# Optimization experiments

Hardware: AMD Instinct MI355X
Metric: run time of the kernel (lower is better)

Reference implementation:

```python
import jax, jax.numpy as jnp
import numpy as np

N = 50000        # vertices
E = 1_600_000    # edges (avg degree 32)
CIN = 8          # in_channels (scalar input features)
COUT = 32        # out_channels (tangent vector channels, complex -> trailing dim 2)
R = 2            # n_corr_rings (radial profile rings)
EPS = 1e-6


def setup_inputs() -> dict:
    key = jax.random.key(0)
    ks = jax.random.split(key, 12)
    x = jax.random.normal(ks[0], (N, CIN), jnp.float32)
    edge_index = jax.random.randint(ks[1], (2, E), 0, N, dtype=jnp.int32)
    # precomputed per-edge transport * radial interpolation coefficients (re, im) per ring
    pcmp_gather = jax.random.normal(ks[2], (E, R, 2), jnp.float32)
    # TransField learned radial profile and phase offset (offset=True)
    W_rad = jax.random.normal(ks[3], (R, CIN, COUT), jnp.float32) / np.float32(np.sqrt(R * CIN))
    phase = jax.random.normal(ks[4], (COUT,), jnp.float32)
    # TangentNonLin bias after the field conv
    b_nl = jax.random.normal(ks[5], (COUT,), jnp.float32) * 0.1
    # three TangentPerceptrons: complex-linear (real weight shared over re/im) + TangentNonLin
    sc = np.float32(1.0 / np.sqrt(COUT))
    W1 = jax.random.normal(ks[6], (COUT, COUT), jnp.float32) * sc
    b1 = jax.random.normal(ks[7], (COUT,), jnp.float32) * 0.1
    W2 = jax.random.normal(ks[8], (COUT, COUT), jnp.float32) * sc
    b2 = jax.random.normal(ks[9], (COUT,), jnp.float32) * 0.1
    W3 = jax.random.normal(ks[10], (COUT, COUT), jnp.float32) * sc
    b3 = jax.random.normal(ks[11], (COUT,), jnp.float32) * 0.1
    return dict(x=x, edge_index=edge_index, pcmp_gather=pcmp_gather, W_rad=W_rad,
                phase=phase, b_nl=b_nl, W1=W1, b1=b1, W2=W2, b2=b2, W3=W3, b3=b3)


def tangent_nonlin(z, b):
    # ReLU on magnitude with learned per-channel bias, phase preserved
    mag = jnp.sqrt(jnp.sum(z * z, axis=-1) + EPS)           # [N, C]
    scale = jax.nn.relu(mag + b) / mag                      # [N, C]
    return z * scale[..., None]


def trans_field(x, src, dst, pcmp_gather, W_rad, phase, n_nodes):
    xs = x[src]                                             # gather: [E, CIN]
    t = jnp.einsum('ei,rio->ero', xs, W_rad)                # [E, R, COUT]
    # modulate by complex transport coeffs per ring, sum rings -> [E, COUT, 2]
    msg = jnp.sum(t[..., None] * pcmp_gather[:, :, None, :], axis=1)
    agg = jax.ops.segment_sum(msg, dst, num_segments=n_nodes)  # scatter: [N, COUT, 2]
    # learned phase offset: rotate each output channel by e^{i*phase}
    c, s = jnp.cos(phase), jnp.sin(phase)
    re = agg[..., 0] * c - agg[..., 1] * s
    im = agg[..., 0] * s + agg[..., 1] * c
    return jnp.stack([re, im], axis=-1)                     # [N, COUT, 2]


def reference(x, edge_index, pcmp_gather, W_rad, phase, b_nl, W1, b1, W2, b2, W3, b3):
    src, dst = edge_index[0], edge_index[1]
    y = trans_field(x, src, dst, pcmp_gather, W_rad, phase, x.shape[0])
    y = tangent_nonlin(y, b_nl)
    for W, b in ((W1, b1), (W2, b2), (W3, b3)):
        y = jnp.einsum('nik,io->nok', y, W)                 # complex-linear (shared real weight)
        y = tangent_nonlin(y, b)
    return y
```

## Files before the change

kernel.cpp:

```cpp
#include <hip/hip_runtime.h>

#define CIN 8
#define COUT 32
#define NR 2
#define EPSF 1e-6f

#define BSH 5
#define BNODES 32
#define NBMAX 2048
#define CHUNK 4096
#define BINT 512
#define BREG (CHUNK / BINT)
#define IDBITS 21
#define IDMASK ((1u << IDBITS) - 1u)
#define SRCMASK 0x03FFFFFFu
#define PSTAGE 1792
#define AREG (PSTAGE / 256)

__device__ __forceinline__ unsigned bf16r(float f) {
    unsigned u = __float_as_uint(f);
    return (u + 0x7FFFu + ((u >> 16) & 1u)) >> 16;
}
__device__ __forceinline__ unsigned pk2(float a, float b) {
    return bf16r(a) | (bf16r(b) << 16);
}
__device__ __forceinline__ float ulo(unsigned w) { return __uint_as_float(w << 16); }
__device__ __forceinline__ float uhi(unsigned w) { return __uint_as_float(w & 0xFFFF0000u); }

__global__ __launch_bounds__(256) void bucket_hist(
    const int* __restrict__ eidx, int* __restrict__ bucketCnt, int E, int nb)
{
    __shared__ int cnt[NBMAX];
    for (int i = threadIdx.x; i < nb; i += 256) cnt[i] = 0;
    __syncthreads();
    for (int e = blockIdx.x * 256 + threadIdx.x; e < E; e += gridDim.x * 256)
        atomicAdd(&cnt[eidx[E + e] >> BSH], 1);
    __syncthreads();
    for (int i = threadIdx.x; i < nb; i += 256)
        if (cnt[i]) atomicAdd(&bucketCnt[i], cnt[i]);
}

__global__ __launch_bounds__(1024) void scan_init(
    const int* __restrict__ bucketCnt, int* __restrict__ bucketBase,
    int* __restrict__ gCursor, int nb)
{
    __shared__ int sA[NBMAX], sB[NBMAX];
    for (int i = threadIdx.x; i < NBMAX; i += 1024)
        sA[i] = (i < nb) ? bucketCnt[i] : 0;
    __syncthreads();
    int* src = sA; int* dst = sB;
    for (int off = 1; off < NBMAX; off <<= 1) {
        for (int i = threadIdx.x; i < NBMAX; i += 1024)
            dst[i] = src[i] + (i >= off ? src[i - off] : 0);
        __syncthreads();
        int* tmp = src; src = dst; dst = tmp;
    }
    for (int i = threadIdx.x; i < nb; i += 1024) {
        int incl = src[i];
        int base = incl - bucketCnt[i];
        bucketBase[i] = base;
        gCursor[i] = base;
        if (i == nb - 1) bucketBase[nb] = incl;
    }
}

template<bool PACKED>
__global__ __launch_bounds__(BINT) void binify(
    const int* __restrict__ eidx, int* __restrict__ gCursor,
    unsigned* __restrict__ outMeta,
    uint2*    __restrict__ pcmpS,
    const float* __restrict__ pcmp, int E, int nb)
{
    __shared__ int cnt[NBMAX];
    __shared__ int sIncl[NBMAX];
    __shared__ int gbase[NBMAX];
    __shared__ int wsum[8];
    __shared__ unsigned sid[CHUNK];
    __shared__ unsigned short bucketOf[CHUNK];

    const int e0 = blockIdx.x * CHUNK;
    const int num = min(CHUNK, E - e0);
    const int t = threadIdx.x;
    const int lane = t & 63, wid = t >> 6;

    for (int i = t; i < nb; i += BINT) cnt[i] = 0;
    __syncthreads();

    int dreg[BREG];
#pragma unroll
    for (int kk = 0; kk < BREG; ++kk) {
        int k = t + kk * BINT;
        if (k < num) {
            dreg[kk] = eidx[E + e0 + k];
            atomicAdd(&cnt[dreg[kk] >> BSH], 1);
        }
    }
    __syncthreads();

    {
        int j0 = t * 4;
        int v0 = (j0 + 0 < nb) ? cnt[j0 + 0] : 0;
        int v1 = (j0 + 1 < nb) ? cnt[j0 + 1] : 0;
        int v2 = (j0 + 2 < nb) ? cnt[j0 + 2] : 0;
        int v3 = (j0 + 3 < nb) ? cnt[j0 + 3] : 0;
        int p0 = v0, p1 = p0 + v1, p2 = p1 + v2, p3 = p2 + v3;
        int incl = p3;
#pragma unroll
        for (int off = 1; off < 64; off <<= 1) {
            int u = __shfl_up(incl, off, 64);
            if (lane >= off) incl += u;
        }
        int laneEx = incl - p3;
        if (lane == 63) wsum[wid] = incl;
        __syncthreads();
        if (t == 0) {
            int acc = 0;
#pragma unroll
            for (int i = 0; i < 8; ++i) { int w = wsum[i]; wsum[i] = acc; acc += w; }
        }
        __syncthreads();
        int off0 = wsum[wid] + laneEx;
        sIncl[j0 + 0] = off0 + p0;
        sIncl[j0 + 1] = off0 + p1;
        sIncl[j0 + 2] = off0 + p2;
        sIncl[j0 + 3] = off0 + p3;
    }
    __syncthreads();

    for (int b = t; b < nb; b += BINT) {
        int c = sIncl[b] - (b ? sIncl[b - 1] : 0);
        gbase[b] = c ? atomicAdd(&gCursor[b], c) : 0;
    }
    __syncthreads();
    for (int i = t; i < nb; i += BINT) cnt[i] = 0;
    __syncthreads();

#pragma unroll
    for (int kk = 0; kk < BREG; ++kk) {
        int k = t + kk * BINT;
        if (k < num) {
            int e = e0 + k;
            int d = dreg[kk];
            int b = d >> BSH;
            int slot = (b ? sIncl[b - 1] : 0) + atomicAdd(&cnt[b], 1);
            sid[slot] = ((unsigned)(d & (BNODES - 1)) << IDBITS) | (unsigned)e;
            bucketOf[slot] = (unsigned short)b;
        }
    }
    __syncthreads();

    for (int s = t; s < num; s += BINT) {
        int b = bucketOf[s];
        int intra = s - (b ? sIncl[b - 1] : 0);
        unsigned v = sid[s];
        int pos = gbase[b] + intra;
        if (PACKED) {
            int id = v & IDMASK;
            unsigned dl = v >> IDBITS;
            unsigned sv = (unsigned)eidx[id];
            outMeta[pos] = (dl << 26) | sv;
            float4 pc = *reinterpret_cast<const float4*>(pcmp + (size_t)id * 4);
            uint2 pw;
            pw.x = pk2(pc.x, pc.y);
            pw.y = pk2(pc.z, pc.w);
            pcmpS[pos] = pw;
        } else {
            outMeta[pos] = v;
        }
    }
}

template<bool SRC16>
__global__ __launch_bounds__(256, 6) void fused_team_kernel(
    const float* __restrict__ x,
    const uint2* __restrict__ pcmpS,
    const unsigned* __restrict__ meta,
    const int* __restrict__ bucketBase,
    const float* __restrict__ W_rad, const float* __restrict__ phase,
    const float* __restrict__ b_nl,
    const float* __restrict__ W1, const float* __restrict__ b1,
    const float* __restrict__ W2, const float* __restrict__ b2,
    const float* __restrict__ W3, const float* __restrict__ b3,
    float* __restrict__ out, int N)
{
    __shared__ float sWrad[NR * CIN][COUT];
    __shared__ float sPh[COUT][2];
    __shared__ float sBias[4][COUT];
    __shared__ unsigned srtPk[PSTAGE];
    __shared__ unsigned short srtK[SRC16 ? 2 : PSTAGE];
    __shared__ float Qbuf[BNODES][33];
    __shared__ int cnt[BNODES], segS[BNODES], cur[BNODES];

    for (int i = threadIdx.x; i < NR * CIN * COUT; i += 256) ((float*)sWrad)[i] = W_rad[i];
    if (threadIdx.x < COUT) {
        float sn, cs; __sincosf(phase[threadIdx.x], &sn, &cs);
        sPh[threadIdx.x][0] = cs; sPh[threadIdx.x][1] = sn;
        sBias[0][threadIdx.x] = b_nl[threadIdx.x];
        sBias[1][threadIdx.x] = b1[threadIdx.x];
        sBias[2][threadIdx.x] = b2[threadIdx.x];
        sBias[3][threadIdx.x] = b3[threadIdx.x];
    }
    if (threadIdx.x < BNODES) cnt[threadIdx.x] = 0;

    const int start = bucketBase[blockIdx.x];
    const int total = bucketBase[blockIdx.x + 1] - start;
    const bool fb = (total > PSTAGE);
    __syncthreads();

    unsigned mreg[AREG];
    const int staged = fb ? 0 : total;
#pragma unroll
    for (int kk = 0; kk < AREG; ++kk) {
        int k = threadIdx.x + (kk << 8);
        if (k < staged) {
            mreg[kk] = meta[start + k];
            atomicAdd(&cnt[mreg[kk] >> 26], 1);
        }
    }
    __syncthreads();

    if (threadIdx.x < BNODES) {
        int v = cnt[threadIdx.x];
        int incl = v;
#pragma unroll
        for (int off = 1; off < BNODES; off <<= 1) {
            int u = __shfl_up(incl, off, 32);
            if ((int)threadIdx.x >= off) incl += u;
        }
        segS[threadIdx.x] = incl - v;
        cur[threadIdx.x]  = incl - v;
    }
    __syncthreads();

    if (!fb) {
#pragma unroll
        for (int kk = 0; kk < AREG; ++kk) {
            int k = threadIdx.x + (kk << 8);
            if (k < staged) {
                unsigned m = mreg[kk];
                int pos = atomicAdd(&cur[m >> 26], 1);
                if (SRC16) {
                    srtPk[pos] = ((unsigned)k << 16) | (m & 0xFFFFu);
                } else {
                    srtPk[pos] = m & SRCMASK;
                    srtK[pos] = (unsigned short)k;
                }
            }
        }
    }
    __syncthreads();

    const int c    = threadIdx.x & 31;
    const int sub  = threadIdx.x >> 5;
    const int team = c >> 3;
    const int il   = c & 7;
    const int gl   = sub * 4 + team;
    const int node0 = blockIdx.x << BSH;

    float4 qa = {0.f, 0.f, 0.f, 0.f};
    if (!fb) {
        const int base  = segS[gl];
        const int myCnt = cnt[gl];
        const uint2* __restrict__ pcb = pcmpS + start;
        int t = 0;
        for (; t + 4 <= myCnt; t += 4) {
            int s0, s1, s2, s3, k0, k1, k2, k3;
            if (SRC16) {
                unsigned p0 = srtPk[base + t],     p1 = srtPk[base + t + 1];
                unsigned p2 = srtPk[base + t + 2], p3 = srtPk[base + t + 3];
                s0 = (int)(p0 & 0xFFFFu); k0 = (int)(p0 >> 16);
                s1 = (int)(p1 & 0xFFFFu); k1 = (int)(p1 >> 16);
                s2 = (int)(p2 & 0xFFFFu); k2 = (int)(p2 >> 16);
                s3 = (int)(p3 & 0xFFFFu); k3 = (int)(p3 >> 16);
            } else {
                s0 = (int)srtPk[base + t];     k0 = srtK[base + t];
                s1 = (int)srtPk[base + t + 1]; k1 = srtK[base + t + 1];
                s2 = (int)srtPk[base + t + 2]; k2 = srtK[base + t + 2];
                s3 = (int)srtPk[base + t + 3]; k3 = srtK[base + t + 3];
            }
            uint2 w0 = pcb[k0];
            uint2 w1 = pcb[k1];
            uint2 w2 = pcb[k2];
            uint2 w3 = pcb[k3];
            float x0 = x[(s0 << 3) + il];
            float x1 = x[(s1 << 3) + il];
            float x2 = x[(s2 << 3) + il];
            float x3 = x[(s3 << 3) + il];
            qa.x += x0 * ulo(w0.x); qa.y += x0 * uhi(w0.x);
            qa.z += x0 * ulo(w0.y); qa.w += x0 * uhi(w0.y);
            qa.x += x1 * ulo(w1.x); qa.y += x1 * uhi(w1.x);
            qa.z += x1 * ulo(w1.y); qa.w += x1 * uhi(w1.y);
            qa.x += x2 * ulo(w2.x); qa.y += x2 * uhi(w2.x);
            qa.z += x2 * ulo(w2.y); qa.w += x2 * uhi(w2.y);
            qa.x += x3 * ulo(w3.x); qa.y += x3 * uhi(w3.x);
            qa.z += x3 * ulo(w3.y); qa.w += x3 * uhi(w3.y);
        }
        for (; t < myCnt; ++t) {
            int sv, kv;
            if (SRC16) {
                unsigned p = srtPk[base + t];
                sv = (int)(p & 0xFFFFu); kv = (int)(p >> 16);
            } else {
                sv = (int)srtPk[base + t]; kv = srtK[base + t];
            }
            uint2 w = pcb[kv];
            float xf = x[(sv << 3) + il];
            qa.x += xf * ulo(w.x); qa.y += xf * uhi(w.x);
            qa.z += xf * ulo(w.y); qa.w += xf * uhi(w.y);
        }
    } else {
        const uint2* pcG = pcmpS + start;
        for (int t = 0; t < total; ++t) {
            unsigned m = meta[start + t];
            if ((int)(m >> 26) == gl) {
                uint2 w = pcG[t];
                float xf = x[(size_t)(m & SRCMASK) * CIN + il];
                qa.x += xf * ulo(w.x); qa.y += xf * uhi(w.x);
                qa.z += xf * ulo(w.y); qa.w += xf * uhi(w.y);
            }
        }
    }

    Qbuf[gl][2 * il]      = qa.x;
    Qbuf[gl][2 * il + 1]  = qa.y;
    Qbuf[gl][16 + 2 * il] = qa.z;
    Qbuf[gl][17 + 2 * il] = qa.w;

#pragma unroll
    for (int r = 0; r < 4; ++r) {
        const int gln = sub * 4 + r;
        const int n   = node0 + gln;
        float a0 = 0.f, a1 = 0.f;
#pragma unroll
        for (int ri = 0; ri < NR * CIN; ++ri) {
            float w = sWrad[ri][c];
            a0 += w * Qbuf[gln][2 * ri];
            a1 += w * Qbuf[gln][2 * ri + 1];
        }
        float cs = sPh[c][0], sn = sPh[c][1];
        float re = a0 * cs - a1 * sn;
        float im = a0 * sn + a1 * cs;
        float mag = sqrtf(re * re + im * im + EPSF);
        float sc  = fmaxf(mag + sBias[0][c], 0.f) / mag;
        re *= sc; im *= sc;
#pragma unroll
        for (int L = 0; L < 3; ++L) {
            const float* __restrict__ Wl = (L == 0) ? W1 : (L == 1) ? W2 : W3;
            float bb0 = 0.f, bb1 = 0.f;
#pragma unroll
            for (int i = 0; i < COUT; ++i) {
                float w = Wl[i * COUT + c];
                bb0 += w * __shfl(re, i, 32);
                bb1 += w * __shfl(im, i, 32);
            }
            float m2 = sqrtf(bb0 * bb0 + bb1 * bb1 + EPSF);
            float s2 = fmaxf(m2 + sBias[L + 1][c], 0.f) / m2;
            re = bb0 * s2; im = bb1 * s2;
        }
        if (n < N) {
            float2 v; v.x = re; v.y = im;
            *reinterpret_cast<float2*>(out + ((n << 6) + (c << 1))) = v;
        }
    }
}

__global__ __launch_bounds__(256) void fused_bucket_fallback(
    const float* __restrict__ x, const int* __restrict__ eidx,
    const float* __restrict__ pcmp, const int* __restrict__ bucketBase,
    const unsigned* __restrict__ sorted,
    const float* __restrict__ W_rad, const float* __restrict__ phase,
    const float* __restrict__ b_nl,
    const float* __restrict__ W1, const float* __restrict__ b1,
    const float* __restrict__ W2, const float* __restrict__ b2,
    const float* __restrict__ W3, const float* __restrict__ b3,
    float* __restrict__ out, int N)
{
    __shared__ float Q[BNODES][COUT];
    __shared__ float sWrad[NR * CIN][COUT];
    __shared__ float sW[3][COUT][COUT];
    __shared__ float sPh[COUT][2];
    __shared__ float sBias[4][COUT];

    for (int i = threadIdx.x; i < BNODES * COUT; i += 256) ((float*)Q)[i] = 0.f;
    for (int i = threadIdx.x; i < NR * CIN * COUT; i += 256) ((float*)sWrad)[i] = W_rad[i];
    for (int i = threadIdx.x; i < COUT * COUT; i += 256) {
        ((float*)sW[0])[i] = W1[i];
        ((float*)sW[1])[i] = W2[i];
        ((float*)sW[2])[i] = W3[i];
    }
    if (threadIdx.x < COUT) {
        float sn, cs; __sincosf(phase[threadIdx.x], &sn, &cs);
        sPh[threadIdx.x][0] = cs; sPh[threadIdx.x][1] = sn;
        sBias[0][threadIdx.x] = b_nl[threadIdx.x];
        sBias[1][threadIdx.x] = b1[threadIdx.x];
        sBias[2][threadIdx.x] = b2[threadIdx.x];
        sBias[3][threadIdx.x] = b3[threadIdx.x];
    }
    __syncthreads();

    const int c   = threadIdx.x & 31;
    const int sub = threadIdx.x >> 5;
    const int i_idx  = (c >> 1) & 7;
    const int pc_off = ((c >> 4) << 1) | (c & 1);
    const int start = bucketBase[blockIdx.x];
    const int end   = bucketBase[blockIdx.x + 1];

    for (int p = start + sub; p < end; p += 8) {
        unsigned v0 = sorted[p];
        int id0 = v0 & IDMASK;
        int s0 = eidx[id0];
        atomicAdd(&Q[v0 >> IDBITS][c],
                  x[(size_t)s0 * CIN + i_idx] * pcmp[(size_t)id0 * 4 + pc_off]);
    }
    __syncthreads();

    const int node0 = blockIdx.x << BSH;
#pragma unroll
    for (int r = 0; r < 4; ++r) {
        const int gl = r * 8 + sub;
        const int n  = node0 + gl;
        float a0 = 0.f, a1 = 0.f;
#pragma unroll
        for (int ri = 0; ri < NR * CIN; ++ri) {
            float w = sWrad[ri][c];
            a0 += w * Q[gl][2 * ri];
            a1 += w * Q[gl][2 * ri + 1];
        }
        float cs = sPh[c][0], sn = sPh[c][1];
        float re = a0 * cs - a1 * sn;
        float im = a0 * sn + a1 * cs;
        float mag = sqrtf(re * re + im * im + EPSF);
        float sc  = fmaxf(mag + sBias[0][c], 0.f) / mag;
        re *= sc; im *= sc;
#pragma unroll
        for (int L = 0; L < 3; ++L) {
            float b0 = 0.f, b1v = 0.f;
#pragma unroll
            for (int i = 0; i < COUT; ++i) {
                float w = sW[L][i][c];
                b0  += w * __shfl(re, i, 32);
                b1v += w * __shfl(im, i, 32);
            }
            float m2 = sqrtf(b0 * b0 + b1v * b1v + EPSF);
            float s2 = fmaxf(m2 + sBias[L + 1][c], 0.f) / m2;
            re = b0 * s2; im = b1v * s2;
        }
        if (n < N) {
            float2 v; v.x = re; v.y = im;
            *reinterpret_cast<float2*>(out + ((size_t)n * COUT + c) * 2) = v;
        }
    }
}

extern "C" void kernel_launch(void* const* d_in, const int* in_sizes, int n_in,
                              void* d_out, int out_size, void* d_ws, size_t ws_size,
                              hipStream_t stream)
{
    const float* x     = (const float*)d_in[0];
    const int*   eidx  = (const int*)  d_in[1];
    const float* pcmp  = (const float*)d_in[2];
    const float* W_rad = (const float*)d_in[3];
    const float* phase = (const float*)d_in[4];
    const float* b_nl  = (const float*)d_in[5];
    const float* W1    = (const float*)d_in[6];
    const float* b1    = (const float*)d_in[7];
    const float* W2    = (const float*)d_in[8];
    const float* b2    = (const float*)d_in[9];
    const float* W3    = (const float*)d_in[10];
    const float* b3    = (const float*)d_in[11];
    float* out = (float*)d_out;

    const int N = in_sizes[0] / CIN;
    const int E = in_sizes[1] / 2;
    const int nb = (N + BNODES - 1) >> BSH;
    const int nchunk = (E + CHUNK - 1) / CHUNK;

    uint2*    pcmpS      = (uint2*)d_ws;
    unsigned* meta       = (unsigned*)(pcmpS + E);
    int*      bucketCnt  = (int*)(meta + E);
    int*      bucketBase = bucketCnt + NBMAX;
    int*      gCursor    = bucketBase + NBMAX + 1;
    size_t needed = (size_t)((char*)(gCursor + NBMAX) - (char*)d_ws);

    if (ws_size >= needed) {
        hipMemsetAsync(bucketCnt, 0, (size_t)nb * sizeof(int), stream);
        bucket_hist<<<256, 256, 0, stream>>>(eidx, bucketCnt, E, nb);
        scan_init<<<1, 1024, 0, stream>>>(bucketCnt, bucketBase, gCursor, nb);
        binify<true><<<nchunk, BINT, 0, stream>>>(eidx, gCursor, meta, pcmpS, pcmp, E, nb);
        if (N <= 65536) {
            fused_team_kernel<true><<<nb, 256, 0, stream>>>(
                x, pcmpS, meta, bucketBase,
                W_rad, phase, b_nl, W1, b1, W2, b2, W3, b3, out, N);
        } else {
            fused_team_kernel<false><<<nb, 256, 0, stream>>>(
                x, pcmpS, meta, bucketBase,
                W_rad, phase, b_nl, W1, b1, W2, b2, W3, b3, out, N);
        }
    } else {
        int*      bc = (int*)d_ws;
        int*      bb = bc + NBMAX;
        int*      gc = bb + NBMAX + 1;
        unsigned* so = (unsigned*)(gc + NBMAX);
        hipMemsetAsync(bc, 0, (size_t)nb * sizeof(int), stream);
        bucket_hist<<<256, 256, 0, stream>>>(eidx, bc, E, nb);
        scan_init<<<1, 1024, 0, stream>>>(bc, bb, gc, nb);
        binify<false><<<nchunk, BINT, 0, stream>>>(eidx, gc, so, nullptr, pcmp, E, nb);
        fused_bucket_fallback<<<nb, 256, 0, stream>>>(
            x, eidx, pcmp, bb, so,
            W_rad, phase, b_nl, W1, b1, W2, b2, W3, b3, out, N);
    }
}
```

Baseline: 164.1 us.

## Stage pcmp coefficients into LDS during counting sort and shuffle-broadcast edges

New measurement: 164.4 us. No clear change (+0.2%).

```diff
diff --git a/kernel.cpp b/kernel.cpp
--- a/kernel.cpp
+++ b/kernel.cpp
@@ -186,8 +186,9 @@
     __shared__ float sWrad[NR * CIN][COUT];
     __shared__ float sPh[COUT][2];
     __shared__ float sBias[4][COUT];
-    __shared__ unsigned srtPk[PSTAGE];
-    __shared__ unsigned short srtK[SRC16 ? 2 : PSTAGE];
+    __shared__ uint2 pcL[PSTAGE];
+    __shared__ unsigned short srtS16[SRC16 ? PSTAGE : 2];
+    __shared__ unsigned srtS32[SRC16 ? 2 : PSTAGE];
     __shared__ float Qbuf[BNODES][33];
     __shared__ int cnt[BNODES], segS[BNODES], cur[BNODES];
 
@@ -208,12 +209,14 @@
     __syncthreads();
 
     unsigned mreg[AREG];
+    uint2    preg[AREG];
     const int staged = fb ? 0 : total;
 #pragma unroll
     for (int kk = 0; kk < AREG; ++kk) {
         int k = threadIdx.x + (kk << 8);
         if (k < staged) {
             mreg[kk] = meta[start + k];
+            preg[kk] = pcmpS[start + k];
             atomicAdd(&cnt[mreg[kk] >> 26], 1);
         }
     }
@@ -239,12 +242,9 @@
             if (k < staged) {
                 unsigned m = mreg[kk];
                 int pos = atomicAdd(&cur[m >> 26], 1);
-                if (SRC16) {
-                    srtPk[pos] = ((unsigned)k << 16) | (m & 0xFFFFu);
-                } else {
-                    srtPk[pos] = m & SRCMASK;
-                    srtK[pos] = (unsigned short)k;
-                }
+                if (SRC16) srtS16[pos] = (unsigned short)(m & 0xFFFFu);
+                else       srtS32[pos] = m & SRCMASK;
+                pcL[pos] = preg[kk];
             }
         }
     }
@@ -254,6 +254,7 @@
     const int sub  = threadIdx.x >> 5;
     const int team = c >> 3;
     const int il   = c & 7;
+    const int tb   = c & 24;
     const int gl   = sub * 4 + team;
     const int node0 = blockIdx.x << BSH;
 
@@ -261,49 +262,26 @@
     if (!fb) {
         const int base  = segS[gl];
         const int myCnt = cnt[gl];
-        const uint2* __restrict__ pcb = pcmpS + start;
         int t = 0;
-        for (; t + 4 <= myCnt; t += 4) {
-            int s0, s1, s2, s3, k0, k1, k2, k3;
-            if (SRC16) {
-                unsigned p0 = srtPk[base + t],     p1 = srtPk[base + t + 1];
-                unsigned p2 = srtPk[base + t + 2], p3 = srtPk[base + t + 3];
-                s0 = (int)(p0 & 0xFFFFu); k0 = (int)(p0 >> 16);
-                s1 = (int)(p1 & 0xFFFFu); k1 = (int)(p1 >> 16);
-                s2 = (int)(p2 & 0xFFFFu); k2 = (int)(p2 >> 16);
-                s3 = (int)(p3 & 0xFFFFu); k3 = (int)(p3 >> 16);
-            } else {
-                s0 = (int)srtPk[base + t];     k0 = srtK[base + t];
-                s1 = (int)srtPk[base + t + 1]; k1 = srtK[base + t + 1];
-                s2 = (int)srtPk[base + t + 2]; k2 = srtK[base + t + 2];
-                s3 = (int)srtPk[base + t + 3]; k3 = srtK[base + t + 3];
+        for (; t + 8 <= myCnt; t += 8) {
+            int e = base + t + il;
+            int svj = SRC16 ? (int)srtS16[e] : (int)srtS32[e];
+            uint2 wj = pcL[e];
+#pragma unroll
+            for (int j = 0; j < 8; ++j) {
+                int src = tb + j;
+                int sv  = __shfl(svj, src, 32);
+                unsigned wx = (unsigned)__shfl((int)wj.x, src, 32);
+                unsigned wy = (unsigned)__shfl((int)wj.y, src, 32);
+                float xf = x[(sv << 3) + il];
+                qa.x += xf * ulo(wx); qa.y += xf * uhi(wx);
+                qa.z += xf * ulo(wy); qa.w += xf * uhi(wy);
             }
-            uint2 w0 = pcb[k0];
-            uint2 w1 = pcb[k1];
-            uint2 w2 = pcb[k2];
-            uint2 w3 = pcb[k3];
-            float x0 = x[(s0 << 3) + il];
-            float x1 = x[(s1 << 3) + il];
-            float x2 = x[(s2 << 3) + il];
-            float x3 = x[(s3 << 3) + il];
-            qa.x += x0 * ulo(w0.x); qa.y += x0 * uhi(w0.x);
-            qa.z += x0 * ulo(w0.y); qa.w += x0 * uhi(w0.y);
-            qa.x += x1 * ulo(w1.x); qa.y += x1 * uhi(w1.x);
-            qa.z += x1 * ulo(w1.y); qa.w += x1 * uhi(w1.y);
-            qa.x += x2 * ulo(w2.x); qa.y += x2 * uhi(w2.x);
-            qa.z += x2 * ulo(w2.y); qa.w += x2 * uhi(w2.y);
-            qa.x += x3 * ulo(w3.x); qa.y += x3 * uhi(w3.x);
-            qa.z += x3 * ulo(w3.y); qa.w += x3 * uhi(w3.y);
         }
         for (; t < myCnt; ++t) {
-            int sv, kv;
-            if (SRC16) {
-                unsigned p = srtPk[base + t];
-                sv = (int)(p & 0xFFFFu); kv = (int)(p >> 16);
-            } else {
-                sv = (int)srtPk[base + t]; kv = srtK[base + t];
-            }
-            uint2 w = pcb[kv];
+            int e = base + t;
+            int sv = SRC16 ? (int)srtS16[e] : (int)srtS32[e];
+            uint2 w = pcL[e];
             float xf = x[(sv << 3) + il];
             qa.x += xf * ulo(w.x); qa.y += xf * uhi(w.x);
             qa.z += xf * ulo(w.y); qa.w += xf * uhi(w.y);
```
